# Optimization experiments

Hardware: AMD Instinct MI355X
Metric: run time of the kernel (lower is better)

## Reference

```python
import jax, jax.numpy as jnp
import numpy as np

N_SRC0, N_DST0 = 400000, 100000
N_DST1 = 25000


def _graph_conv(x_src, src, dst, n_dst, W, b):
    # DGL GraphConv, norm='both': h_v = d_in(v)^-1/2 * sum_{u->v} d_out(u)^-1/2 * x_u @ W + b
    ones = jnp.ones(src.shape[0], dtype=x_src.dtype)
    out_deg = jax.ops.segment_sum(ones, src, num_segments=x_src.shape[0])
    in_deg = jax.ops.segment_sum(ones, dst, num_segments=n_dst)
    cs = jnp.where(out_deg > 0, out_deg ** -0.5, 0.0).astype(x_src.dtype)
    cd = jnp.where(in_deg > 0, in_deg ** -0.5, 0.0).astype(x_src.dtype)
    msg = (x_src * cs[:, None])[src]                      # [E, d_in] gather
    agg = jax.ops.segment_sum(msg, dst, num_segments=n_dst)  # [n_dst, d_in] scatter-add
    return (agg * cd[:, None]) @ W + b


def setup_inputs() -> dict:
    key = jax.random.key(0)
    ks = jax.random.split(key, 8)
    E0, E1 = 3200000, 800000
    return {
        "x": jax.random.normal(ks[0], (N_SRC0, 128), dtype=jnp.float32),
        "src0": jax.random.randint(ks[1], (E0,), 0, N_SRC0, dtype=jnp.int32),
        "dst0": jax.random.randint(ks[2], (E0,), 0, N_DST0, dtype=jnp.int32),
        "src1": jax.random.randint(ks[3], (E1,), 0, N_DST0, dtype=jnp.int32),
        "dst1": jax.random.randint(ks[4], (E1,), 0, N_DST1, dtype=jnp.int32),
        "W0": jax.random.normal(ks[5], (128, 256), dtype=jnp.float32) * (128 ** -0.5),
        "b0": jnp.zeros((256,), dtype=jnp.float32),
        "W1": jax.random.normal(ks[6], (256, 64), dtype=jnp.float32) * (256 ** -0.5),
        "b1": jnp.zeros((64,), dtype=jnp.float32),
    }


def reference(x, src0, dst0, src1, dst1, W0, b0, W1, b1):
    h = jax.nn.relu(_graph_conv(x, src0, dst0, N_DST0, W0, b0))   # [N_DST0, 256]
    h = jax.nn.relu(_graph_conv(h, src1, dst1, N_DST1, W1, b1))   # [N_DST1, 64]
    return h
```

## Files before the change

kernel.cpp:

```cpp
#include <hip/hip_runtime.h>
#include <hip/hip_bf16.h>
#include <hip/hip_fp16.h>
#include <stdint.h>

#define N_SRC0 400000
#define N_DST0 100000
#define N_DST1 25000

#define SH_D0 9
#define NK_D0 196
#define SH_S0 9
#define NK_S0 782
#define SH_D1 8
#define NK_D1 98
#define SH_S1 9
#define NK_S1 196
#define NB0 1024
#define NB1 256

#define BH_D0 0
#define BH_S0 (NK_D0 * NB0)
#define BH_D1 (BH_S0 + NK_S0 * NB0)
#define BH_S1 (BH_D1 + NK_D1 * NB1)
#define BH_TOT (BH_S1 + NK_S1 * NB1)

typedef __attribute__((ext_vector_type(8))) short short8;
typedef __attribute__((ext_vector_type(4))) float f32x4;

__device__ __forceinline__ unsigned short f2bf(float f) {
    __hip_bfloat16 h = __float2bfloat16(f);
    union { __hip_bfloat16 h; unsigned short u; } c;
    c.h = h;
    return c.u;
}
__device__ __forceinline__ uint32_t packbf2(float a, float b) {
    return (uint32_t)f2bf(a) | ((uint32_t)f2bf(b) << 16);
}
__device__ __forceinline__ __half2 u2h2(uint32_t u) {
    return __builtin_bit_cast(__half2, u);
}

__device__ __forceinline__ void hist_body(
        const int* __restrict__ src, const int* __restrict__ dst, int n,
        int sshift, int snb, int dshift, int dnb, int NB, int blk,
        int* __restrict__ bhd, int* __restrict__ bhs, int* h) {
    for (int i = threadIdx.x; i < dnb + snb; i += 256) h[i] = 0;
    __syncthreads();
    const int per = (n + NB - 1) / NB;
    const int b = blk * per;
    const int e = min(b + per, n);
    for (int i = b + threadIdx.x; i < e; i += 256) {
        atomicAdd(&h[dst[i] >> dshift], 1);
        atomicAdd(&h[dnb + (src[i] >> sshift)], 1);
    }
    __syncthreads();
    for (int i = threadIdx.x; i < dnb; i += 256) bhd[(size_t)i * NB + blk] = h[i];
    for (int i = threadIdx.x; i < snb; i += 256) bhs[(size_t)i * NB + blk] = h[dnb + i];
}

__global__ __launch_bounds__(256) void hist_fused(
        const int* __restrict__ src0, const int* __restrict__ dst0, int E0,
        const int* __restrict__ src1, const int* __restrict__ dst1, int E1,
        int* __restrict__ bh) {
    extern __shared__ int h[];
    if (blockIdx.x < NB0)
        hist_body(src0, dst0, E0, SH_S0, NK_S0, SH_D0, NK_D0, NB0, blockIdx.x,
                  bh + BH_D0, bh + BH_S0, h);
    else
        hist_body(src1, dst1, E1, SH_S1, NK_S1, SH_D1, NK_D1, NB1, blockIdx.x - NB0,
                  bh + BH_D1, bh + BH_S1, h);
}

#define SCAN_ITEMS 8
#define SCAN_TILE 2048

__global__ __launch_bounds__(256) void scan1_kernel(
        const int* __restrict__ in, int* __restrict__ out,
        int* __restrict__ sums, int n) {
    __shared__ int lds[256];
    const int tid = threadIdx.x;
    const int base = blockIdx.x * SCAN_TILE + tid * SCAN_ITEMS;
    int v[SCAN_ITEMS];
    int run = 0;
    #pragma unroll
    for (int i = 0; i < SCAN_ITEMS; ++i) {
        int t = (base + i < n) ? in[base + i] : 0;
        v[i] = run;
        run += t;
    }
    lds[tid] = run;
    __syncthreads();
    int incl = run;
    for (int off = 1; off < 256; off <<= 1) {
        int u = (tid >= off) ? lds[tid - off] : 0;
        __syncthreads();
        incl += u;
        lds[tid] = incl;
        __syncthreads();
    }
    if (tid == 255) sums[blockIdx.x] = incl;
    int excl = incl - run;
    #pragma unroll
    for (int i = 0; i < SCAN_ITEMS; ++i)
        if (base + i < n) out[base + i] = excl + v[i];
}

__global__ __launch_bounds__(256) void scan2_kernel(int* __restrict__ sums, int nb) {
    __shared__ int lds[256];
    const int tid = threadIdx.x;
    const int base = tid * 4;
    int v[4];
    int run = 0;
    #pragma unroll
    for (int i = 0; i < 4; ++i) {
        int t = (base + i < nb) ? sums[base + i] : 0;
        v[i] = run;
        run += t;
    }
    lds[tid] = run;
    __syncthreads();
    int incl = run;
    for (int off = 1; off < 256; off <<= 1) {
        int u = (tid >= off) ? lds[tid - off] : 0;
        __syncthreads();
        incl += u;
        lds[tid] = incl;
        __syncthreads();
    }
    int excl = incl - run;
    #pragma unroll
    for (int i = 0; i < 4; ++i)
        if (base + i < nb) sums[base + i] = excl + v[i];
}

__global__ void scan3_kernel(int* __restrict__ out, const int* __restrict__ sums, int n) {
    int i = blockIdx.x * blockDim.x + threadIdx.x;
    if (i < n) out[i] += sums[i / SCAN_TILE];
}

__device__ __forceinline__ void scat_body(
        const int* __restrict__ src, const int* __restrict__ dst, int n,
        int sshift, int snb, int dshift, int dnb, int NB, int blk, int ksh,
        const int* __restrict__ bhd, const int* __restrict__ bhs,
        uint32_t* __restrict__ stg, int* cur) {
    for (int i = threadIdx.x; i < dnb; i += 256) cur[i] = bhd[(size_t)i * NB + blk];
    for (int i = threadIdx.x; i < snb; i += 256) cur[dnb + i] = bhs[(size_t)i * NB + blk];
    __syncthreads();
    const int per = (n + NB - 1) / NB;
    const int b = blk * per;
    const int e = min(b + per, n);
    const int dmask = (1 << dshift) - 1;
    for (int i = b + threadIdx.x; i < e; i += 256) {
        int s = src[i], d = dst[i];
        int pd = atomicAdd(&cur[d >> dshift], 1);
        stg[pd] = ((uint32_t)(d & dmask) << ksh) | (uint32_t)s;
        int ps = atomicAdd(&cur[dnb + (s >> sshift)], 1);
        stg[ps] = (uint32_t)s;
    }
}

__global__ __launch_bounds__(256) void scat_fused(
        const int* __restrict__ src0, const int* __restrict__ dst0, int E0,
        const int* __restrict__ src1, const int* __restrict__ dst1, int E1,
        const int* __restrict__ bh, uint32_t* __restrict__ stg) {
    extern __shared__ int cur[];
    if (blockIdx.x < NB0)
        scat_body(src0, dst0, E0, SH_S0, NK_S0, SH_D0, NK_D0, NB0, blockIdx.x, 19,
                  bh + BH_D0, bh + BH_S0, stg, cur);
    else
        scat_body(src1, dst1, E1, SH_S1, NK_S1, SH_D1, NK_D1, NB1, blockIdx.x - NB0, 17,
                  bh + BH_D1, bh + BH_S1, stg, cur);
}

__device__ __forceinline__ void fine_csr_body(
        const uint32_t* __restrict__ stg, const int* __restrict__ bht,
        int NB, int shift, int ksh, int nbins, int total, int rel, int nbkt, int k,
        int* __restrict__ off, int* __restrict__ esrc, int* fine, int* part) {
    const int fb = 1 << shift;
    const int base = bht[(size_t)k * NB];
    const int end = (k + 1 < nbkt) ? bht[(size_t)(k + 1) * NB] : total;
    const int gb = k << shift;
    const int t = threadIdx.x;
    const uint32_t mask = (1u << ksh) - 1;
    for (int i = t; i < fb; i += 256) fine[i] = 0;
    __syncthreads();
    for (int i = base + t; i < end; i += 256)
        atomicAdd(&fine[stg[i] >> ksh], 1);
    __syncthreads();
    int a0 = (2 * t < fb) ? fine[2 * t] : 0;
    int a1 = (2 * t + 1 < fb) ? fine[2 * t + 1] : 0;
    part[t] = a0 + a1;
    __syncthreads();
    int incl = part[t];
    for (int o = 1; o < 256; o <<= 1) {
        int u = (t >= o) ? part[t - o] : 0;
        __syncthreads();
        incl += u;
        part[t] = incl;
        __syncthreads();
    }
    int excl = incl - (a0 + a1);
    if (2 * t < fb) fine[2 * t] = excl;
    if (2 * t + 1 < fb) fine[2 * t + 1] = excl + a0;
    __syncthreads();
    const int rb = base - rel;
    for (int i = t; i < fb; i += 256) {
        int g = gb + i;
        if (g < nbins) off[g] = rb + fine[i];
    }
    if (k == nbkt - 1 && t == 0) off[nbins] = total - rel;
    __syncthreads();
    for (int i = base + t; i < end; i += 256) {
        uint32_t v = stg[i];
        int p = atomicAdd(&fine[v >> ksh], 1);
        esrc[rb + p] = (int)(v & mask);
    }
}

__device__ __forceinline__ void fine_deg_body(
        const uint32_t* __restrict__ stg, const int* __restrict__ bht,
        int NB, int shift, int nbins, int total, int nbkt, int k,
        uint32_t* __restrict__ csp, float* __restrict__ csf, int* fine) {
    const int fb = 1 << shift;
    const int base = bht[(size_t)k * NB];
    const int end = (k + 1 < nbkt) ? bht[(size_t)(k + 1) * NB] : total;
    const int gb = k << shift;
    for (int i = threadIdx.x; i < fb; i += 256) fine[i] = 0;
    __syncthreads();
    for (int i = base + threadIdx.x; i < end; i += 256)
        atomicAdd(&fine[(int)stg[i] - gb], 1);
    __syncthreads();
    for (int i = threadIdx.x; i < fb; i += 256) {
        int g = gb + i;
        if (g < nbins) {
            int c = fine[i];
            float r = c > 0 ? rsqrtf((float)c) : 0.f;
            if (csp) {
                __half2 h = __floats2half2_rn(r, r);
                csp[g] = __builtin_bit_cast(uint32_t, h);
            } else {
                csf[g] = r;
            }
        }
    }
}

__global__ __launch_bounds__(256) void fine_fused(
        const uint32_t* __restrict__ stg, const int* __restrict__ bh,
        int E0, int E1,
        int* __restrict__ off0, int* __restrict__ esrc0,
        int* __restrict__ off1, int* __restrict__ esrc1,
        uint32_t* __restrict__ cs0p, float* __restrict__ cs1) {
    __shared__ int fine[512];
    __shared__ int part[256];
    int kb = blockIdx.x;
    if (kb < NK_D0) {
        fine_csr_body(stg, bh + BH_D0, NB0, SH_D0, 19, N_DST0, E0, 0, NK_D0, kb,
                      off0, esrc0, fine, part);
        return;
    }
    kb -= NK_D0;
    if (kb < NK_S0) {
        fine_deg_body(stg, bh + BH_S0, NB0, SH_S0, N_SRC0, 2 * E0, NK_S0, kb,
                      cs0p, nullptr, fine);
        return;
    }
    kb -= NK_S0;
    if (kb < NK_D1) {
        fine_csr_body(stg, bh + BH_D1, NB1, SH_D1, 17, N_DST1, 2 * E0 + E1, 2 * E0, NK_D1, kb,
                      off1, esrc1, fine, part);
        return;
    }
    kb -= NK_D1;
    fine_deg_body(stg, bh + BH_S1, NB1, SH_S1, N_DST0, 2 * E0 + 2 * E1, NK_S1, kb,
                  nullptr, cs1, fine);
}

__global__ __launch_bounds__(256) void xconv_kernel(
        const float4* __restrict__ x4, uint2* __restrict__ xs) {
    int id = blockIdx.x * 256 + threadIdx.x;
    float4 v = x4[id];
    uint2 o;
    o.x = __builtin_bit_cast(uint32_t, __floats2half2_rn(v.x, v.y));
    o.y = __builtin_bit_cast(uint32_t, __floats2half2_rn(v.z, v.w));
    xs[id] = o;
}

__global__ __launch_bounds__(256) void packw_fused(
        const float* __restrict__ W0, const float* __restrict__ W1,
        unsigned short* __restrict__ W0p, unsigned short* __restrict__ W1p) {
    int blk = blockIdx.x;
    if (blk < 128) {
        int id = blk * 256 + threadIdx.x;
        int kk = id & 31, n2 = (id >> 5) & 255, kt = id >> 13;
        W0p[id] = f2bf(W0[(kt * 32 + kk) * 256 + n2]);
    } else {
        int id = (blk - 128) * 256 + threadIdx.x;
        int kk = id & 31, n2 = (id >> 5) & 63, kt = id >> 11;
        W1p[id] = f2bf(W1[(kt * 32 + kk) * 64 + n2]);
    }
}

__global__ __launch_bounds__(256) void agg0_kernel(
        const uint4* __restrict__ xs4, const int* __restrict__ esrc,
        const int* __restrict__ off, const uint32_t* __restrict__ cs0p,
        uint4* __restrict__ aggb4) {
    const int row = blockIdx.x * 16 + (threadIdx.x >> 4);
    const int t = threadIdx.x & 15;
    const int b = off[row], e = off[row + 1];
    const __half2 z = __builtin_bit_cast(__half2, 0u);
    __half2 aA0 = z, aA1 = z, aA2 = z, aA3 = z;
    __half2 aB0 = z, aB1 = z, aB2 = z, aB3 = z;
    int i = b;
    for (; i + 8 <= e; i += 8) {
        #pragma unroll
        for (int k = 0; k < 8; k += 2) {
            int s0 = esrc[i + k], s1 = esrc[i + k + 1];
            __half2 c0 = u2h2(cs0p[s0]), c1 = u2h2(cs0p[s1]);
            uint4 v0 = xs4[(size_t)s0 * 16 + t];
            uint4 v1 = xs4[(size_t)s1 * 16 + t];
            aA0 = __hfma2(u2h2(v0.x), c0, aA0);
            aA1 = __hfma2(u2h2(v0.y), c0, aA1);
            aA2 = __hfma2(u2h2(v0.z), c0, aA2);
            aA3 = __hfma2(u2h2(v0.w), c0, aA3);
            aB0 = __hfma2(u2h2(v1.x), c1, aB0);
            aB1 = __hfma2(u2h2(v1.y), c1, aB1);
            aB2 = __hfma2(u2h2(v1.z), c1, aB2);
            aB3 = __hfma2(u2h2(v1.w), c1, aB3);
        }
    }
    for (; i < e; ++i) {
        int s = esrc[i];
        __half2 c = u2h2(cs0p[s]);
        uint4 v = xs4[(size_t)s * 16 + t];
        aA0 = __hfma2(u2h2(v.x), c, aA0);
        aA1 = __hfma2(u2h2(v.y), c, aA1);
        aA2 = __hfma2(u2h2(v.z), c, aA2);
        aA3 = __hfma2(u2h2(v.w), c, aA3);
    }
    float cd = (e > b) ? rsqrtf((float)(e - b)) : 0.f;
    __half2 s0 = __hadd2(aA0, aB0), s1 = __hadd2(aA1, aB1);
    __half2 s2 = __hadd2(aA2, aB2), s3 = __hadd2(aA3, aB3);
    uint4 o;
    o.x = packbf2(__low2float(s0) * cd, __high2float(s0) * cd);
    o.y = packbf2(__low2float(s1) * cd, __high2float(s1) * cd);
    o.z = packbf2(__low2float(s2) * cd, __high2float(s2) * cd);
    o.w = packbf2(__low2float(s3) * cd, __high2float(s3) * cd);
    aggb4[(size_t)row * 16 + t] = o;
}

__global__ __launch_bounds__(256) void gemm0_mfma(
        const short* __restrict__ A,
        const short* __restrict__ Bp,
        const float* __restrict__ bias,
        unsigned short* __restrict__ H) {
    const int w = threadIdx.x >> 6;
    const int l = threadIdx.x & 63;
    const int rbase = blockIdx.x * 32;
    const int cbase = w * 64;
    const int lr = l & 15;
    const int lk = (l >> 4) * 8;
    f32x4 acc[2][4] = {};
    #pragma unroll
    for (int kt = 0; kt < 4; ++kt) {
        short8 a[2], b[4];
        #pragma unroll
        for (int rt = 0; rt < 2; ++rt)
            a[rt] = *(const short8*)(A + (size_t)(rbase + rt * 16 + lr) * 128 + kt * 32 + lk);
        #pragma unroll
        for (int ct = 0; ct < 4; ++ct)
            b[ct] = *(const short8*)(Bp + (size_t)(kt * 256 + cbase + ct * 16 + lr) * 32 + lk);
        #pragma unroll
        for (int rt = 0; rt < 2; ++rt)
            #pragma unroll
            for (int ct = 0; ct < 4; ++ct)
                acc[rt][ct] = __builtin_amdgcn_mfma_f32_16x16x32_bf16(a[rt], b[ct], acc[rt][ct], 0, 0, 0);
    }
    const int orow0 = (l >> 4) * 4;
    #pragma unroll
    for (int rt = 0; rt < 2; ++rt) {
        #pragma unroll
        for (int ct = 0; ct < 4; ++ct) {
            int col = cbase + ct * 16 + lr;
            float bv = bias[col];
            #pragma unroll
            for (int j = 0; j < 4; ++j) {
                int row = rbase + rt * 16 + orow0 + j;
                float v = fmaxf(acc[rt][ct][j] + bv, 0.f);
                H[(size_t)row * 256 + col] = f2bf(v);
            }
        }
    }
}

__global__ __launch_bounds__(256) void gemmt_mfma(
        const short* __restrict__ A,
        const short* __restrict__ Bp,
        const float* __restrict__ cs1,
        __half* __restrict__ Y,
        int M) {
    const int w = threadIdx.x >> 6;
    const int l = threadIdx.x & 63;
    const int rbase = blockIdx.x * 128 + w * 32;
    const int lr = l & 15;
    const int lk = (l >> 4) * 8;
    f32x4 acc[2][4] = {};
    #pragma unroll
    for (int kt = 0; kt < 8; ++kt) {
        short8 a[2], b[4];
        #pragma unroll
        for (int rt = 0; rt < 2; ++rt)
            a[rt] = *(const short8*)(A + (size_t)(rbase + rt * 16 + lr) * 256 + kt * 32 + lk);
        #pragma unroll
        for (int ct = 0; ct < 4; ++ct)
            b[ct] = *(const short8*)(Bp + (size_t)(kt * 64 + ct * 16 + lr) * 32 + lk);
        #pragma unroll
        for (int rt = 0; rt < 2; ++rt)
            #pragma unroll
            for (int ct = 0; ct < 4; ++ct)
                acc[rt][ct] = __builtin_amdgcn_mfma_f32_16x16x32_bf16(a[rt], b[ct], acc[rt][ct], 0, 0, 0);
    }
    const int orow0 = (l >> 4) * 4;
    #pragma unroll
    for (int rt = 0; rt < 2; ++rt) {
        #pragma unroll
        for (int j = 0; j < 4; ++j) {
            int row = rbase + rt * 16 + orow0 + j;
            if (row < M) {
                float c = cs1[row];
                #pragma unroll
                for (int ct = 0; ct < 4; ++ct) {
                    int col = ct * 16 + lr;
                    Y[(size_t)row * 64 + col] = __float2half(acc[rt][ct][j] * c);
                }
            }
        }
    }
}

__global__ __launch_bounds__(256) void agg1_kernel(
        const uint2* __restrict__ y2, const int* __restrict__ esrc,
        const int* __restrict__ off, const float* __restrict__ bias,
        float* __restrict__ out, int nrows) {
    int row = blockIdx.x * 16 + (threadIdx.x >> 4);
    int t = threadIdx.x & 15;
    if (row >= nrows) return;
    int b = off[row], e = off[row + 1];
    const __half2 z = __builtin_bit_cast(__half2, 0u);
    __half2 aA0 = z, aA1 = z, aB0 = z, aB1 = z;
    int i = b;
    for (; i + 8 <= e; i += 8) {
        #pragma unroll
        for (int k = 0; k < 8; k += 2) {
            int s0 = esrc[i + k], s1 = esrc[i + k + 1];
            uint2 v0 = y2[(size_t)s0 * 16 + t];
            uint2 v1 = y2[(size_t)s1 * 16 + t];
            aA0 = __hadd2(aA0, u2h2(v0.x));
            aA1 = __hadd2(aA1, u2h2(v0.y));
            aB0 = __hadd2(aB0, u2h2(v1.x));
            aB1 = __hadd2(aB1, u2h2(v1.y));
        }
    }
    for (; i < e; ++i) {
        uint2 v = y2[(size_t)esrc[i] * 16 + t];
        aA0 = __hadd2(aA0, u2h2(v.x));
        aA1 = __hadd2(aA1, u2h2(v.y));
    }
    float cd = (e > b) ? rsqrtf((float)(e - b)) : 0.f;
    __half2 s0 = __hadd2(aA0, aB0), s1 = __hadd2(aA1, aB1);
    float4 bv = *(const float4*)(bias + t * 4);
    float4 o;
    o.x = fmaxf(__low2float(s0) * cd + bv.x, 0.f);
    o.y = fmaxf(__high2float(s0) * cd + bv.y, 0.f);
    o.z = fmaxf(__low2float(s1) * cd + bv.z, 0.f);
    o.w = fmaxf(__high2float(s1) * cd + bv.w, 0.f);
    *(float4*)(out + (size_t)row * 64 + t * 4) = o;
}

extern "C" void kernel_launch(void* const* d_in, const int* in_sizes, int n_in,
                              void* d_out, int out_size, void* d_ws, size_t ws_size,
                              hipStream_t stream) {
    const float* x    = (const float*)d_in[0];
    const int*   src0 = (const int*)d_in[1];
    const int*   dst0 = (const int*)d_in[2];
    const int*   src1 = (const int*)d_in[3];
    const int*   dst1 = (const int*)d_in[4];
    const float* W0   = (const float*)d_in[5];
    const float* b0   = (const float*)d_in[6];
    const float* W1   = (const float*)d_in[7];
    const float* b1   = (const float*)d_in[8];
    float* out = (float*)d_out;

    const int E0 = in_sizes[1];
    const int E1 = in_sizes[3];
    const int M_PAD = 100096;

    char* p = (char*)d_ws;
    auto alloc = [&](size_t bytes) {
        char* r = p;
        p += (bytes + 511) & ~(size_t)511;
        return r;
    };
    int*      bh    = (int*)alloc((size_t)BH_TOT * 4);
    int*      sums  = (int*)alloc(1024 * 4);
    int*      off0  = (int*)alloc((size_t)(N_DST0 + 1) * 4);
    int*      off1  = (int*)alloc((size_t)(N_DST1 + 1) * 4);
    uint32_t* cs0p  = (uint32_t*)alloc((size_t)N_SRC0 * 4);
    float*    cs1   = (float*)alloc((size_t)N_DST0 * 4);
    int*      esrc0 = (int*)alloc((size_t)E0 * 4);
    int*      esrc1 = (int*)alloc((size_t)E1 * 4);
    unsigned short* W0p = (unsigned short*)alloc((size_t)32768 * 2);
    unsigned short* W1p = (unsigned short*)alloc((size_t)16384 * 2);
    size_t bigA = (size_t)N_SRC0 * 128 * 2;
    size_t bigB = (size_t)N_DST0 * 128 * 2;
    size_t bigStg = (size_t)(2 * E0 + 2 * E1) * 4;
    size_t bigSz = bigA + bigB;
    if (bigStg > bigSz) bigSz = bigStg;
    char* big = alloc(bigSz);

    uint32_t* stg = (uint32_t*)big;
    uint2*    xs  = (uint2*)big;
    unsigned short* h0b = (unsigned short*)big;
    char* regB = big + bigA;
    uint4* aggb4 = (uint4*)regB;
    __half* y1b  = (__half*)regB;

    hist_fused<<<NB0 + NB1, 256, (NK_D0 + NK_S0) * 4, stream>>>(
        src0, dst0, E0, src1, dst1, E1, bh);
    const int nsb = (BH_TOT + SCAN_TILE - 1) / SCAN_TILE;
    scan1_kernel<<<nsb, 256, 0, stream>>>(bh, bh, sums, BH_TOT);
    scan2_kernel<<<1, 256, 0, stream>>>(sums, nsb);
    scan3_kernel<<<(BH_TOT + 255) / 256, 256, 0, stream>>>(bh, sums, BH_TOT);
    scat_fused<<<NB0 + NB1, 256, (NK_D0 + NK_S0) * 4, stream>>>(
        src0, dst0, E0, src1, dst1, E1, bh, stg);
    fine_fused<<<NK_D0 + NK_S0 + NK_D1 + NK_S1, 256, 0, stream>>>(
        stg, bh, E0, E1, off0, esrc0, off1, esrc1, cs0p, cs1);

    packw_fused<<<192, 256, 0, stream>>>(W0, W1, W0p, W1p);
    xconv_kernel<<<N_SRC0 * 32 / 256, 256, 0, stream>>>((const float4*)x, xs);

    agg0_kernel<<<N_DST0 / 16, 256, 0, stream>>>(
        (const uint4*)xs, esrc0, off0, cs0p, aggb4);
    gemm0_mfma<<<N_DST0 / 32, 256, 0, stream>>>(
        (const short*)aggb4, (const short*)W0p, b0, h0b);

    gemmt_mfma<<<M_PAD / 128, 256, 0, stream>>>(
        (const short*)h0b, (const short*)W1p, cs1, y1b, N_DST0);
    agg1_kernel<<<(N_DST1 + 15) / 16, 256, 0, stream>>>(
        (const uint2*)y1b, esrc1, off1, b1, out, N_DST1);
}
```

Baseline: 436.6 us.

## Prescale source features by out-degree and fuse both GEMMs via LDS

The source-side normalisation is folded into the fp32-to-fp16 conversion kernel, so the layer-0 aggregation only sums gathered rows and no longer gathers a per-edge scale. The aggregation now gives each row a full 64-lane wave reading 4-byte chunks, with eight independent accumulators. Layer 0's GEMM and the layer-1 transform GEMM are fused into one kernel that keeps the ReLU'd bf16 hidden tile in shared memory, removing the global write and reread of the 100k x 256 intermediate. The trade-offs are narrower per-lane loads in the gather and extra LDS use plus a barrier in the fused GEMM.

```diff
diff --git a/kernel.cpp b/kernel.cpp
--- a/kernel.cpp
+++ b/kernel.cpp
@@ -220,7 +220,7 @@
 __device__ __forceinline__ void fine_deg_body(
         const uint32_t* __restrict__ stg, const int* __restrict__ bht,
         int NB, int shift, int nbins, int total, int nbkt, int k,
-        uint32_t* __restrict__ csp, float* __restrict__ csf, int* fine) {
+        float* __restrict__ csf, int* fine) {
     const int fb = 1 << shift;
     const int base = bht[(size_t)k * NB];
     const int end = (k + 1 < nbkt) ? bht[(size_t)(k + 1) * NB] : total;
@@ -234,13 +234,7 @@
         int g = gb + i;
         if (g < nbins) {
             int c = fine[i];
-            float r = c > 0 ? rsqrtf((float)c) : 0.f;
-            if (csp) {
-                __half2 h = __floats2half2_rn(r, r);
-                csp[g] = __builtin_bit_cast(uint32_t, h);
-            } else {
-                csf[g] = r;
-            }
+            csf[g] = c > 0 ? rsqrtf((float)c) : 0.f;
         }
     }
 }
@@ -250,7 +244,7 @@
         int E0, int E1,
         int* __restrict__ off0, int* __restrict__ esrc0,
         int* __restrict__ off1, int* __restrict__ esrc1,
-        uint32_t* __restrict__ cs0p, float* __restrict__ cs1) {
+        float* __restrict__ cs0, float* __restrict__ cs1) {
     __shared__ int fine[512];
     __shared__ int part[256];
     int kb = blockIdx.x;
@@ -262,7 +256,7 @@
     kb -= NK_D0;
     if (kb < NK_S0) {
         fine_deg_body(stg, bh + BH_S0, NB0, SH_S0, N_SRC0, 2 * E0, NK_S0, kb,
-                      cs0p, nullptr, fine);
+                      cs0, fine);
         return;
     }
     kb -= NK_S0;
@@ -273,16 +267,19 @@
     }
     kb -= NK_D1;
     fine_deg_body(stg, bh + BH_S1, NB1, SH_S1, N_DST0, 2 * E0 + 2 * E1, NK_S1, kb,
-                  nullptr, cs1, fine);
-}
-
-__global__ __launch_bounds__(256) void xconv_kernel(
-        const float4* __restrict__ x4, uint2* __restrict__ xs) {
+                  cs1, fine);
+}
+
+__global__ __launch_bounds__(256) void prescale_kernel(
+        const float4* __restrict__ x4, const float* __restrict__ cs,
+        uint2* __restrict__ xs) {
     int id = blockIdx.x * 256 + threadIdx.x;
+    int row = id >> 5;
+    float c = cs[row];
     float4 v = x4[id];
     uint2 o;
-    o.x = __builtin_bit_cast(uint32_t, __floats2half2_rn(v.x, v.y));
-    o.y = __builtin_bit_cast(uint32_t, __floats2half2_rn(v.z, v.w));
+    o.x = __builtin_bit_cast(uint32_t, __floats2half2_rn(v.x * c, v.y * c));
+    o.y = __builtin_bit_cast(uint32_t, __floats2half2_rn(v.z * c, v.w * c));
     xs[id] = o;
 }
 
@@ -302,137 +299,99 @@
 }
 
 __global__ __launch_bounds__(256) void agg0_kernel(
-        const uint4* __restrict__ xs4, const int* __restrict__ esrc,
-        const int* __restrict__ off, const uint32_t* __restrict__ cs0p,
-        uint4* __restrict__ aggb4) {
-    const int row = blockIdx.x * 16 + (threadIdx.x >> 4);
-    const int t = threadIdx.x & 15;
+        const uint32_t* __restrict__ xs, const int* __restrict__ esrc,
+        const int* __restrict__ off, uint32_t* __restrict__ aggb) {
+    const int row = blockIdx.x * 4 + (threadIdx.x >> 6);
+    const int t = threadIdx.x & 63;
     const int b = off[row], e = off[row + 1];
     const __half2 z = __builtin_bit_cast(__half2, 0u);
-    __half2 aA0 = z, aA1 = z, aA2 = z, aA3 = z;
-    __half2 aB0 = z, aB1 = z, aB2 = z, aB3 = z;
+    __half2 a0 = z, a1 = z, a2 = z, a3 = z, a4 = z, a5 = z, a6 = z, a7 = z;
     int i = b;
-    for (; i + 8 <= e; i += 8) {
-        #pragma unroll
-        for (int k = 0; k < 8; k += 2) {
-            int s0 = esrc[i + k], s1 = esrc[i + k + 1];
-            __half2 c0 = u2h2(cs0p[s0]), c1 = u2h2(cs0p[s1]);
-            uint4 v0 = xs4[(size_t)s0 * 16 + t];
-            uint4 v1 = xs4[(size_t)s1 * 16 + t];
-            aA0 = __hfma2(u2h2(v0.x), c0, aA0);
-            aA1 = __hfma2(u2h2(v0.y), c0, aA1);
-            aA2 = __hfma2(u2h2(v0.z), c0, aA2);
-            aA3 = __hfma2(u2h2(v0.w), c0, aA3);
-            aB0 = __hfma2(u2h2(v1.x), c1, aB0);
-            aB1 = __hfma2(u2h2(v1.y), c1, aB1);
-            aB2 = __hfma2(u2h2(v1.z), c1, aB2);
-            aB3 = __hfma2(u2h2(v1.w), c1, aB3);
-        }
-    }
-    for (; i < e; ++i) {
-        int s = esrc[i];
-        __half2 c = u2h2(cs0p[s]);
-        uint4 v = xs4[(size_t)s * 16 + t];
-        aA0 = __hfma2(u2h2(v.x), c, aA0);
-        aA1 = __hfma2(u2h2(v.y), c, aA1);
-        aA2 = __hfma2(u2h2(v.z), c, aA2);
-        aA3 = __hfma2(u2h2(v.w), c, aA3);
-    }
+    for (; i + 7 < e; i += 8) {
+        int s0 = esrc[i],     s1 = esrc[i + 1], s2 = esrc[i + 2], s3 = esrc[i + 3];
+        int s4 = esrc[i + 4], s5 = esrc[i + 5], s6 = esrc[i + 6], s7 = esrc[i + 7];
+        a0 = __hadd2(a0, u2h2(xs[(size_t)s0 * 64 + t]));
+        a1 = __hadd2(a1, u2h2(xs[(size_t)s1 * 64 + t]));
+        a2 = __hadd2(a2, u2h2(xs[(size_t)s2 * 64 + t]));
+        a3 = __hadd2(a3, u2h2(xs[(size_t)s3 * 64 + t]));
+        a4 = __hadd2(a4, u2h2(xs[(size_t)s4 * 64 + t]));
+        a5 = __hadd2(a5, u2h2(xs[(size_t)s5 * 64 + t]));
+        a6 = __hadd2(a6, u2h2(xs[(size_t)s6 * 64 + t]));
+        a7 = __hadd2(a7, u2h2(xs[(size_t)s7 * 64 + t]));
+    }
+    for (; i < e; ++i)
+        a0 = __hadd2(a0, u2h2(xs[(size_t)esrc[i] * 64 + t]));
+    __half2 s = __hadd2(__hadd2(__hadd2(a0, a1), __hadd2(a2, a3)),
+                        __hadd2(__hadd2(a4, a5), __hadd2(a6, a7)));
     float cd = (e > b) ? rsqrtf((float)(e - b)) : 0.f;
-    __half2 s0 = __hadd2(aA0, aB0), s1 = __hadd2(aA1, aB1);
-    __half2 s2 = __hadd2(aA2, aB2), s3 = __hadd2(aA3, aB3);
-    uint4 o;
-    o.x = packbf2(__low2float(s0) * cd, __high2float(s0) * cd);
-    o.y = packbf2(__low2float(s1) * cd, __high2float(s1) * cd);
-    o.z = packbf2(__low2float(s2) * cd, __high2float(s2) * cd);
-    o.w = packbf2(__low2float(s3) * cd, __high2float(s3) * cd);
-    aggb4[(size_t)row * 16 + t] = o;
-}
-
-__global__ __launch_bounds__(256) void gemm0_mfma(
+    aggb[(size_t)row * 64 + t] = packbf2(__low2float(s) * cd, __high2float(s) * cd);
+}
+
+__global__ __launch_bounds__(256) void gemm01_mfma(
         const short* __restrict__ A,
-        const short* __restrict__ Bp,
-        const float* __restrict__ bias,
-        unsigned short* __restrict__ H) {
+        const short* __restrict__ B0p,
+        const float* __restrict__ bias0,
+        const short* __restrict__ B1p,
+        const float* __restrict__ cs1,
+        __half* __restrict__ Y) {
+    __shared__ short hs[32][272];
     const int w = threadIdx.x >> 6;
     const int l = threadIdx.x & 63;
     const int rbase = blockIdx.x * 32;
-    const int cbase = w * 64;
     const int lr = l & 15;
     const int lk = (l >> 4) * 8;
-    f32x4 acc[2][4] = {};
-    #pragma unroll
-    for (int kt = 0; kt < 4; ++kt) {
-        short8 a[2], b[4];
+    const int orow0 = (l >> 4) * 4;
+
+    {
+        const int cbase = w * 64;
+        f32x4 acc[2][4] = {};
         #pragma unroll
-        for (int rt = 0; rt < 2; ++rt)
-            a[rt] = *(const short8*)(A + (size_t)(rbase + rt * 16 + lr) * 128 + kt * 32 + lk);
-        #pragma unroll
-        for (int ct = 0; ct < 4; ++ct)
-            b[ct] = *(const short8*)(Bp + (size_t)(kt * 256 + cbase + ct * 16 + lr) * 32 + lk);
-        #pragma unroll
-        for (int rt = 0; rt < 2; ++rt)
+        for (int kt = 0; kt < 4; ++kt) {
+            short8 a[2], b[4];
+            #pragma unroll
+            for (int rt = 0; rt < 2; ++rt)
+                a[rt] = *(const short8*)(A + (size_t)(rbase + rt * 16 + lr) * 128 + kt * 32 + lk);
             #pragma unroll
             for (int ct = 0; ct < 4; ++ct)
-                acc[rt][ct] = __builtin_amdgcn_mfma_f32_16x16x32_bf16(a[rt], b[ct], acc[rt][ct], 0, 0, 0);
-    }
-    const int orow0 = (l >> 4) * 4;
-    #pragma unroll
-    for (int rt = 0; rt < 2; ++rt) {
+                b[ct] = *(const short8*)(B0p + (size_t)(kt * 256 + cbase + ct * 16 + lr) * 32 + lk);
+            #pragma unroll
+            for (int rt = 0; rt < 2; ++rt)
+                #pragma unroll
+                for (int ct = 0; ct < 4; ++ct)
+                    acc[rt][ct] = __builtin_amdgcn_mfma_f32_16x16x32_bf16(a[rt], b[ct], acc[rt][ct], 0, 0, 0);
+        }
         #pragma unroll
-        for (int ct = 0; ct < 4; ++ct) {
-            int col = cbase + ct * 16 + lr;
-            float bv = bias[col];
+        for (int rt = 0; rt < 2; ++rt) {
+            #pragma unroll
+            for (int ct = 0; ct < 4; ++ct) {
+                int col = cbase + ct * 16 + lr;
+                float bv = bias0[col];
+                #pragma unroll
+                for (int j = 0; j < 4; ++j)
+                    hs[rt * 16 + orow0 + j][col] = (short)f2bf(fmaxf(acc[rt][ct][j] + bv, 0.f));
+            }
+        }
+    }
+    __syncthreads();
+
+    {
+        f32x4 acc2[2] = {};
+        #pragma unroll
+        for (int kt = 0; kt < 8; ++kt) {
+            short8 b1 = *(const short8*)(B1p + (size_t)(kt * 64 + w * 16 + lr) * 32 + lk);
+            #pragma unroll
+            for (int rt = 0; rt < 2; ++rt) {
+                short8 av = *(const short8*)(&hs[rt * 16 + lr][kt * 32 + lk]);
+                acc2[rt] = __builtin_amdgcn_mfma_f32_16x16x32_bf16(av, b1, acc2[rt], 0, 0, 0);
+            }
+        }
+        #pragma unroll
+        for (int rt = 0; rt < 2; ++rt) {
             #pragma unroll
             for (int j = 0; j < 4; ++j) {
                 int row = rbase + rt * 16 + orow0 + j;
-                float v = fmaxf(acc[rt][ct][j] + bv, 0.f);
-                H[(size_t)row * 256 + col] = f2bf(v);
-            }
-        }
-    }
-}
-
-__global__ __launch_bounds__(256) void gemmt_mfma(
-        const short* __restrict__ A,
-        const short* __restrict__ Bp,
-        const float* __restrict__ cs1,
-        __half* __restrict__ Y,
-        int M) {
-    const int w = threadIdx.x >> 6;
-    const int l = threadIdx.x & 63;
-    const int rbase = blockIdx.x * 128 + w * 32;
-    const int lr = l & 15;
-    const int lk = (l >> 4) * 8;
-    f32x4 acc[2][4] = {};
-    #pragma unroll
-    for (int kt = 0; kt < 8; ++kt) {
-        short8 a[2], b[4];
-        #pragma unroll
-        for (int rt = 0; rt < 2; ++rt)
-            a[rt] = *(const short8*)(A + (size_t)(rbase + rt * 16 + lr) * 256 + kt * 32 + lk);
-        #pragma unroll
-        for (int ct = 0; ct < 4; ++ct)
-            b[ct] = *(const short8*)(Bp + (size_t)(kt * 64 + ct * 16 + lr) * 32 + lk);
-        #pragma unroll
-        for (int rt = 0; rt < 2; ++rt)
-            #pragma unroll
-            for (int ct = 0; ct < 4; ++ct)
-                acc[rt][ct] = __builtin_amdgcn_mfma_f32_16x16x32_bf16(a[rt], b[ct], acc[rt][ct], 0, 0, 0);
-    }
-    const int orow0 = (l >> 4) * 4;
-    #pragma unroll
-    for (int rt = 0; rt < 2; ++rt) {
-        #pragma unroll
-        for (int j = 0; j < 4; ++j) {
-            int row = rbase + rt * 16 + orow0 + j;
-            if (row < M) {
                 float c = cs1[row];
-                #pragma unroll
-                for (int ct = 0; ct < 4; ++ct) {
-                    int col = ct * 16 + lr;
-                    Y[(size_t)row * 64 + col] = __float2half(acc[rt][ct][j] * c);
-                }
+                Y[(size_t)row * 64 + w * 16 + lr] = __float2half(acc2[rt][j] * c);
             }
         }
     }
@@ -493,7 +452,6 @@
 
     const int E0 = in_sizes[1];
     const int E1 = in_sizes[3];
-    const int M_PAD = 100096;
 
     char* p = (char*)d_ws;
     auto alloc = [&](size_t bytes) {
@@ -501,14 +459,14 @@
         p += (bytes + 511) & ~(size_t)511;
         return r;
     };
-    int*      bh    = (int*)alloc((size_t)BH_TOT * 4);
-    int*      sums  = (int*)alloc(1024 * 4);
-    int*      off0  = (int*)alloc((size_t)(N_DST0 + 1) * 4);
-    int*      off1  = (int*)alloc((size_t)(N_DST1 + 1) * 4);
-    uint32_t* cs0p  = (uint32_t*)alloc((size_t)N_SRC0 * 4);
-    float*    cs1   = (float*)alloc((size_t)N_DST0 * 4);
-    int*      esrc0 = (int*)alloc((size_t)E0 * 4);
-    int*      esrc1 = (int*)alloc((size_t)E1 * 4);
+    int*   bh    = (int*)alloc((size_t)BH_TOT * 4);
+    int*   sums  = (int*)alloc(1024 * 4);
+    int*   off0  = (int*)alloc((size_t)(N_DST0 + 1) * 4);
+    int*   off1  = (int*)alloc((size_t)(N_DST1 + 1) * 4);
+    float* cs0   = (float*)alloc((size_t)N_SRC0 * 4);
+    float* cs1   = (float*)alloc((size_t)N_DST0 * 4);
+    int*   esrc0 = (int*)alloc((size_t)E0 * 4);
+    int*   esrc1 = (int*)alloc((size_t)E1 * 4);
     unsigned short* W0p = (unsigned short*)alloc((size_t)32768 * 2);
     unsigned short* W1p = (unsigned short*)alloc((size_t)16384 * 2);
     size_t bigA = (size_t)N_SRC0 * 128 * 2;
@@ -518,12 +476,10 @@
     if (bigStg > bigSz) bigSz = bigStg;
     char* big = alloc(bigSz);
 
-    uint32_t* stg = (uint32_t*)big;
-    uint2*    xs  = (uint2*)big;
-    unsigned short* h0b = (unsigned short*)big;
-    char* regB = big + bigA;
-    uint4* aggb4 = (uint4*)regB;
-    __half* y1b  = (__half*)regB;
+    uint32_t* stg  = (uint32_t*)big;
+    uint2*    xs   = (uint2*)big;
+    __half*   y1b  = (__half*)big;
+    uint32_t* aggb = (uint32_t*)(big + bigA);
 
     hist_fused<<<NB0 + NB1, 256, (NK_D0 + NK_S0) * 4, stream>>>(
         src0, dst0, E0, src1, dst1, E1, bh);
@@ -534,18 +490,17 @@
     scat_fused<<<NB0 + NB1, 256, (NK_D0 + NK_S0) * 4, stream>>>(
         src0, dst0, E0, src1, dst1, E1, bh, stg);
     fine_fused<<<NK_D0 + NK_S0 + NK_D1 + NK_S1, 256, 0, stream>>>(
-        stg, bh, E0, E1, off0, esrc0, off1, esrc1, cs0p, cs1);
+        stg, bh, E0, E1, off0, esrc0, off1, esrc1, cs0, cs1);
 
     packw_fused<<<192, 256, 0, stream>>>(W0, W1, W0p, W1p);
-    xconv_kernel<<<N_SRC0 * 32 / 256, 256, 0, stream>>>((const float4*)x, xs);
-
-    agg0_kernel<<<N_DST0 / 16, 256, 0, stream>>>(
-        (const uint4*)xs, esrc0, off0, cs0p, aggb4);
-    gemm0_mfma<<<N_DST0 / 32, 256, 0, stream>>>(
-        (const short*)aggb4, (const short*)W0p, b0, h0b);
-
-    gemmt_mfma<<<M_PAD / 128, 256, 0, stream>>>(
-        (const short*)h0b, (const short*)W1p, cs1, y1b, N_DST0);
+    prescale_kernel<<<N_SRC0 * 32 / 256, 256, 0, stream>>>((const float4*)x, cs0, xs);
+
+    agg0_kernel<<<N_DST0 / 4, 256, 0, stream>>>(
+        (const uint32_t*)xs, esrc0, off0, aggb);
+
+    gemm01_mfma<<<N_DST0 / 32, 256, 0, stream>>>(
+        (const short*)aggb, (const short*)W0p, b0, (const short*)W1p, cs1, y1b);
+
     agg1_kernel<<<(N_DST1 + 15) / 16, 256, 0, stream>>>(
         (const uint2*)y1b, esrc1, off1, b1, out, N_DST1);
 }
```

Result: faster. 397.6 us (-8.9%).
